# Optimization experiments

Measured on AMD Instinct MI355X. Metric: run time of the kernel, lower is better.

Reference implementation:

```python
import jax, jax.numpy as jnp
import numpy as np

D = 512      # d_model
S = 8        # num_quantum_states
B, T = 16, 1024
LN_EPS = 1e-5


def setup_inputs() -> dict:
    key = jax.random.key(0)
    ks = jax.random.split(key, 10)
    sc = lambda fan_in: 1.0 / np.sqrt(fan_in)
    return {
        "x": jax.random.normal(ks[0], (B, T, D), dtype=jnp.float32),
        # entanglement gates: torch Linear weight [out=D, in=2D], bias [D], stacked over S
        "W_ent": jax.random.uniform(ks[1], (S, D, 2 * D), minval=-sc(2 * D), maxval=sc(2 * D)),
        "b_ent": jax.random.uniform(ks[2], (S, D), minval=-sc(2 * D), maxval=sc(2 * D)),
        # measurement MLP: Linear(D*S->D), LayerNorm(D), Tanh, Linear(D->1)
        "m1_w": jax.random.uniform(ks[3], (D, D * S), minval=-sc(D * S), maxval=sc(D * S)),
        "m1_b": jax.random.uniform(ks[4], (D,), minval=-sc(D * S), maxval=sc(D * S)),
        "ln_g": jnp.ones((D,), dtype=jnp.float32),
        "ln_b": jnp.zeros((D,), dtype=jnp.float32),
        "m2_w": jax.random.uniform(ks[5], (1, D), minval=-sc(D), maxval=sc(D)),
        "m2_b": jax.random.uniform(ks[6], (1,), minval=-sc(D), maxval=sc(D)),
    }


def _layernorm(h, g, b):
    mu = jnp.mean(h, axis=-1, keepdims=True)
    var = jnp.mean(jnp.square(h - mu), axis=-1, keepdims=True)
    return (h - mu) * jax.lax.rsqrt(var + LN_EPS) * g + b


def reference(x, W_ent, b_ent, m1_w, m1_b, ln_g, ln_b, m2_w, m2_b):
    b_, t_, d_ = x.shape
    s_ = W_ent.shape[0]
    # gate(cat[x_i, x_j]).mean(dim=2) == x_i @ W1^T + mean_j(x_j) @ W2^T + b  (exact algebra)
    W1 = W_ent[:, :, :d_]   # [S, D, D] acts on x_i
    W2 = W_ent[:, :, d_:]   # [S, D, D] acts on x_j (mean over j)
    xbar = jnp.mean(x, axis=1)                                   # [B, D]
    ent = (jnp.einsum('btd,sed->bste', x, W1)                    # [B, S, T, D]
           + jnp.einsum('bd,sed->bse', xbar, W2)[:, :, None, :]
           + b_ent[None, :, None, :])
    # permute(0,2,3,1).reshape(B,T,D*S): feature layout is (d, s) fastest on s
    qv = jnp.transpose(ent, (0, 2, 3, 1)).reshape(b_, t_, d_ * s_)
    h = jnp.tanh(_layernorm(qv @ m1_w.T + m1_b, ln_g, ln_b))     # [B, T, D]
    attn_logits = h @ m2_w.T + m2_b                              # [B, T, 1]
    attn_weights = jax.nn.softmax(attn_logits, axis=1)
    context = jnp.sum(attn_weights * x, axis=1)                  # [B, D]
    return context, attn_weights
```

## Files before the change

### kernel.cpp

```cpp
#include <hip/hip_runtime.h>
#include <hip/hip_bf16.h>

typedef __attribute__((ext_vector_type(8))) short bf16x8;
typedef __attribute__((ext_vector_type(4))) float f32x4;

__device__ __forceinline__ float bf2f(unsigned short u) {
    union { unsigned int i; float f; } c; c.i = ((unsigned int)u) << 16; return c.f;
}
__device__ __forceinline__ unsigned short f2bf(float f) {
    union { float f; unsigned int i; } c; c.f = f;
    unsigned int x = c.i;
    x += 0x7fffu + ((x >> 16) & 1u);
    return (unsigned short)(x >> 16);
}
__device__ __forceinline__ unsigned int pk2(float a, float b) {
    __hip_bfloat162 h = __float22bfloat162_rn(float2{a, b});
    union { __hip_bfloat162 h; unsigned int u; } c; c.h = h; return c.u;
}
__device__ __forceinline__ float tanh_fast(float v) {
    float a = fabsf(v);
    a = fminf(a, 15.0f);
    float e = __expf(2.0f * a);
    float t = 1.0f - 2.0f / (e + 1.0f);
    return copysignf(t, v);
}

#define GLOAD_LDS16(gp, lp) \
    __builtin_amdgcn_global_load_lds((const __attribute__((address_space(1))) void*)(gp), \
                                     (__attribute__((address_space(3))) void*)(lp), 16, 0, 0)

#define MFMA(a, b, c) __builtin_amdgcn_mfma_f32_16x16x32_bf16((a), (b), (c), 0, 0, 0)

#define SBAR()  __builtin_amdgcn_s_barrier()
#define SCHED0() __builtin_amdgcn_sched_barrier(0)


__global__ void k_sumxp(const float* __restrict__ x, float* __restrict__ sumxp) {
    int b = blockIdx.x, tc = blockIdx.y;
    int tid = threadIdx.x;
    const float* xp = x + ((size_t)b * 1024 + tc * 64) * 512;
    float a0 = 0.f, a1 = 0.f;
    for (int t = 0; t < 64; ++t) {
        a0 += xp[(size_t)t * 512 + tid];
        a1 += xp[(size_t)t * 512 + tid + 256];
    }
    float* o = sumxp + (size_t)(b * 16 + tc) * 512;
    o[tid] = a0;
    o[tid + 256] = a1;
}

__global__ void k_prepA(const float* __restrict__ m1w, const float* __restrict__ bent,
                        unsigned short* __restrict__ Abf, float* __restrict__ bias2) {
    int i = blockIdx.x, tid = threadIdx.x;
    const float* row = m1w + (size_t)i * 4096;
    float acc = 0.f;
    #pragma unroll
    for (int q = 0; q < 4; ++q) {
        int col = q * 1024 + tid * 4;
        float4 v = *(const float4*)(row + col);
        ushort4 o;
        o.x = f2bf(v.x); o.y = f2bf(v.y); o.z = f2bf(v.z); o.w = f2bf(v.w);
        *(ushort4*)(Abf + (size_t)i * 4096 + col) = o;
        int e0 = col >> 3, s0 = col & 7;
        acc += v.x * bent[(s0    ) * 512 + e0];
        acc += v.y * bent[(s0 + 1) * 512 + e0];
        acc += v.z * bent[(s0 + 2) * 512 + e0];
        acc += v.w * bent[(s0 + 3) * 512 + e0];
    }
    #pragma unroll
    for (int off = 32; off; off >>= 1) acc += __shfl_xor(acc, off);
    __shared__ float r4[4];
    if ((tid & 63) == 0) r4[tid >> 6] = acc;
    __syncthreads();
    if (tid == 0) bias2[i] = r4[0] + r4[1] + r4[2] + r4[3];
}

__global__ void k_conv_W(const float* __restrict__ W, unsigned short* __restrict__ WT) {
    __shared__ float tile[128][33];
    int e0 = blockIdx.x * 16;
    int j0 = blockIdx.y * 32;
    int tid = threadIdx.x;
    int tx = tid & 31, ty = tid >> 5;
    #pragma unroll
    for (int q = 0; q < 16; ++q) {
        int lk = q * 8 + ty;
        int de = lk >> 3, s = lk & 7;
        int r = s * 512 + e0 + de;
        tile[lk][tx] = W[(size_t)r * 1024 + j0 + tx];
    }
    __syncthreads();
    int j = tid >> 3, ck = (tid & 7) * 16;
    unsigned short* dst = WT + (size_t)(j0 + j) * 4096 + e0 * 8 + ck;
    #pragma unroll
    for (int g = 0; g < 4; ++g) {
        ushort4 o;
        o.x = f2bf(tile[ck + g * 4 + 0][j]);
        o.y = f2bf(tile[ck + g * 4 + 1][j]);
        o.z = f2bf(tile[ck + g * 4 + 2][j]);
        o.w = f2bf(tile[ck + g * 4 + 3][j]);
        *(ushort4*)(dst + g * 4) = o;
    }
}

__launch_bounds__(512, 2)
__global__ void k_gemm1(const unsigned short* __restrict__ Abf,
                        const unsigned short* __restrict__ WT,
                        float* __restrict__ CpL, float* __restrict__ CpR) {
    __shared__ __align__(16) unsigned short sA[2][64 * 64];
    __shared__ __align__(16) unsigned short sB[2][256 * 64];
    int i0 = blockIdx.x * 64;
    int j0 = blockIdx.y * 256;
    int kbase = blockIdx.z * 512;
    int tid = threadIdx.x, lane = tid & 63, w = tid >> 6;
    int wm = w >> 2, wn = w & 3;
    int lr = lane >> 3, sl = lane & 7;
    int lo = lane & 15, hi = lane >> 4;
    int arow = w * 8 + lr;
    const unsigned short* gA = Abf + (size_t)(i0 + arow) * 4096 + kbase + ((sl ^ lr) << 3);
    const unsigned short* gB0 = WT + (size_t)(j0 + w * 32 + 0 * 8 + lr) * 4096 + kbase + ((sl ^ lr) << 3);
    const unsigned short* gB1 = WT + (size_t)(j0 + w * 32 + 1 * 8 + lr) * 4096 + kbase + ((sl ^ lr) << 3);
    const unsigned short* gB2 = WT + (size_t)(j0 + w * 32 + 2 * 8 + lr) * 4096 + kbase + ((sl ^ lr) << 3);
    const unsigned short* gB3 = WT + (size_t)(j0 + w * 32 + 3 * 8 + lr) * 4096 + kbase + ((sl ^ lr) << 3);
    bool left = (blockIdx.y < 2);
    f32x4 acc[2][4] = {};

#define G1_STAGE(tt, bufn)                                                    \
    do {                                                                      \
        int koff = (tt) * 64;                                                 \
        GLOAD_LDS16(gA + koff, &sA[bufn][w * 8 * 64]);                        \
        GLOAD_LDS16(gB0 + koff, &sB[bufn][(w * 32 + 0) * 64]);                \
        GLOAD_LDS16(gB1 + koff, &sB[bufn][(w * 32 + 8) * 64]);                \
        GLOAD_LDS16(gB2 + koff, &sB[bufn][(w * 32 + 16) * 64]);               \
        GLOAD_LDS16(gB3 + koff, &sB[bufn][(w * 32 + 24) * 64]);               \
        SCHED0();                                                             \
    } while (0)

    G1_STAGE(0, 0);
    #pragma unroll
    for (int t = 0; t < 8; ++t) {
        int buf = t & 1;
        if (t < 7) {
            G1_STAGE(t + 1, buf ^ 1);
            asm volatile("s_waitcnt vmcnt(5)" ::: "memory");
        } else {
            asm volatile("s_waitcnt vmcnt(0)" ::: "memory");
        }
        SCHED0(); SBAR(); SCHED0();
        __builtin_amdgcn_s_setprio(1);
        #pragma unroll
        for (int kk = 0; kk < 2; ++kk) {
            int slotX = ((kk * 4 + hi) ^ (lo & 7)) << 3;
            bf16x8 a0 = *(const bf16x8*)(&sA[buf][(wm * 32 +      lo) * 64 + slotX]);
            bf16x8 a1 = *(const bf16x8*)(&sA[buf][(wm * 32 + 16 + lo) * 64 + slotX]);
            #pragma unroll
            for (int n = 0; n < 4; ++n) {
                bf16x8 bb = *(const bf16x8*)(&sB[buf][(wn * 64 + n * 16 + lo) * 64 + slotX]);
                if (left) {
                    acc[0][n] = MFMA(a0, bb, acc[0][n]);
                    acc[1][n] = MFMA(a1, bb, acc[1][n]);
                } else {
                    acc[0][n] = MFMA(bb, a0, acc[0][n]);
                    acc[1][n] = MFMA(bb, a1, acc[1][n]);
                }
            }
        }
        __builtin_amdgcn_s_setprio(0);
        if (t < 7) { SCHED0(); SBAR(); SCHED0(); }
    }
#undef G1_STAGE

    int ksoff = blockIdx.z * 262144;
    if (left) {
        #pragma unroll
        for (int m = 0; m < 2; ++m) {
            int ib = i0 + wm * 32 + m * 16 + hi * 4;
            #pragma unroll
            for (int n = 0; n < 4; ++n) {
                int j = j0 + wn * 64 + n * 16 + lo;
                #pragma unroll
                for (int r = 0; r < 4; ++r)
                    CpL[ksoff + (ib + r) * 512 + j] = acc[m][n][r];
            }
        }
    } else {
        #pragma unroll
        for (int m = 0; m < 2; ++m) {
            int ic = i0 + wm * 32 + m * 16 + lo;
            #pragma unroll
            for (int n = 0; n < 4; ++n) {
                int db = j0 - 512 + wn * 64 + n * 16 + hi * 4;
                #pragma unroll
                for (int r = 0; r < 4; ++r)
                    CpR[ksoff + (db + r) * 512 + ic] = acc[m][n][r];
            }
        }
    }
}

__global__ void k_reduce(const float* __restrict__ CpL, const float* __restrict__ CpR,
                         unsigned short* __restrict__ M1bf, unsigned short* __restrict__ M2t) {
    int bx = blockIdx.x;
    const float* Cp = (bx < 256) ? CpL : CpR;
    unsigned short* ob = (bx < 256) ? M1bf : M2t;
    int gid = (bx & 255) * 256 + threadIdx.x;
    float4 s = ((const float4*)Cp)[gid];
    #pragma unroll
    for (int ks = 1; ks < 8; ++ks) {
        float4 t = ((const float4*)Cp)[ks * 65536 + gid];
        s.x += t.x; s.y += t.y; s.z += t.z; s.w += t.w;
    }
    ushort4 o;
    o.x = f2bf(s.x); o.y = f2bf(s.y); o.z = f2bf(s.z); o.w = f2bf(s.w);
    ((ushort4*)ob)[gid] = o;
}

__global__ void k_cb(const float* __restrict__ sumxp, const unsigned short* __restrict__ M2t,
                     const float* __restrict__ bias2, const float* __restrict__ m1b,
                     float* __restrict__ cbo) {
    int b = blockIdx.x, i0 = blockIdx.y * 64;
    int tid = threadIdx.x;
    __shared__ float sSx[512];
    for (int d = tid; d < 512; d += 256) {
        float s = 0.f;
        #pragma unroll
        for (int p = 0; p < 16; ++p)
            s += sumxp[(size_t)(b * 16 + p) * 512 + d];
        sSx[d] = s;
    }
    __syncthreads();
    int il = tid & 63, dq = tid >> 6;
    const unsigned short* mp = M2t + (size_t)dq * 128 * 512 + i0 + il;
    float acc = 0.f;
    #pragma unroll 4
    for (int dd = 0; dd < 128; ++dd)
        acc += sSx[dq * 128 + dd] * bf2f(mp[(size_t)dd * 512]);
    __shared__ float sPart[4][64];
    sPart[dq][il] = acc;
    __syncthreads();
    if (tid < 64) {
        float v = sPart[0][tid] + sPart[1][tid] + sPart[2][tid] + sPart[3][tid];
        cbo[b * 512 + i0 + tid] = v * (1.0f / 1024.0f) + bias2[i0 + tid] + m1b[i0 + tid];
    }
}

__launch_bounds__(512)
__global__ void k_gemm2s(const float* __restrict__ x,
                         const unsigned short* __restrict__ M1bf,
                         unsigned short* __restrict__ ypk) {
    __shared__ __align__(16) unsigned short sA[64 * 64];
    __shared__ __align__(16) unsigned short sB[512 * 64];
    int bt0 = blockIdx.x * 64;
    int tid = threadIdx.x, lane = tid & 63, w = tid >> 6;
    int wm = w >> 2, wn = w & 3;
    int lo = lane & 15, hi = lane >> 4;
    int lr = lane >> 3, sl = lane & 7;
    int arow = tid >> 3, aslot = tid & 7;
    const float* gA = x + (size_t)(bt0 + arow) * 512 + aslot * 8;
    unsigned short* dAp = sA + arow * 64 + ((aslot ^ (arow & 7)) << 3);
    const unsigned short* gB[8];
    #pragma unroll
    for (int g = 0; g < 8; ++g)
        gB[g] = M1bf + (size_t)(w * 64 + g * 8 + lr) * 512 + ((sl ^ lr) << 3);
    f32x4 acc[2][8] = {};
    for (int k0 = 0; k0 < 512; k0 += 64) {
        if (k0) __syncthreads();
        #pragma unroll
        for (int g = 0; g < 8; ++g)
            GLOAD_LDS16(gB[g] + k0, &sB[(w * 64 + g * 8) * 64]);
        float4 f0 = *(const float4*)(gA + k0);
        float4 f1 = *(const float4*)(gA + k0 + 4);
        bf16x8 pk;
        pk[0] = (short)f2bf(f0.x); pk[1] = (short)f2bf(f0.y);
        pk[2] = (short)f2bf(f0.z); pk[3] = (short)f2bf(f0.w);
        pk[4] = (short)f2bf(f1.x); pk[5] = (short)f2bf(f1.y);
        pk[6] = (short)f2bf(f1.z); pk[7] = (short)f2bf(f1.w);
        *(bf16x8*)dAp = pk;
        __syncthreads();
        #pragma unroll
        for (int kk = 0; kk < 2; ++kk) {
            int slotX = ((kk * 4 + hi) ^ (lo & 7)) << 3;
            bf16x8 a0 = *(const bf16x8*)(sA + (wm * 32 +      lo) * 64 + slotX);
            bf16x8 a1 = *(const bf16x8*)(sA + (wm * 32 + 16 + lo) * 64 + slotX);
            #pragma unroll
            for (int n = 0; n < 8; ++n) {
                bf16x8 bb = *(const bf16x8*)(sB + (wn * 128 + n * 16 + lo) * 64 + slotX);
                acc[0][n] = MFMA(a0, bb, acc[0][n]);
                acc[1][n] = MFMA(a1, bb, acc[1][n]);
            }
        }
    }
    unsigned short* yb = ypk + (size_t)blockIdx.x * 32768;
    #pragma unroll
    for (int m = 0; m < 2; ++m) {
        #pragma unroll
        for (int n = 0; n < 8; ++n) {
            unsigned int u0 = pk2(acc[m][n][0], acc[m][n][1]);
            unsigned int u1 = pk2(acc[m][n][2], acc[m][n][3]);
            uint2 o; o.x = u0; o.y = u1;
            *(uint2*)(yb + (((w * 16 + m * 8 + n) << 8) + (lane << 2))) = o;
        }
    }
}

__launch_bounds__(512)
__global__ void k_lnlogit(const unsigned short* __restrict__ ypk,
                          const float* __restrict__ cb,
                          const float* __restrict__ lng, const float* __restrict__ lnb,
                          const float* __restrict__ m2w, const float* __restrict__ m2b,
                          float* __restrict__ logits) {
    __shared__ __align__(16) unsigned short sY[32768];
    __shared__ float sCb[512], sG[512], sBe[512], sW[512];
    __shared__ float sS1[64][8], sS2[64][8], sLg[64][8];
    int blk = blockIdx.x;
    int bt0 = blk * 64;
    int b = bt0 >> 10;
    int tid = threadIdx.x, w = tid >> 6, lane = tid & 63;
    sCb[tid] = cb[b * 512 + tid];
    sG[tid]  = lng[tid];
    sBe[tid] = lnb[tid];
    sW[tid]  = m2w[tid];
    const unsigned short* src = ypk + (size_t)blk * 32768;
    #pragma unroll
    for (int it = 0; it < 8; ++it) {
        int off = (w * 8 + it) * 512;
        GLOAD_LDS16(src + off + (lane << 3), &sY[off]);
    }
    asm volatile("s_waitcnt vmcnt(0)" ::: "memory");
    __syncthreads();

    int row = tid >> 3, sub = tid & 7;
    int wm = row >> 5, m = (row >> 4) & 1, hi = (row >> 2) & 3, r = row & 3;
    float s1 = 0.f, s2 = 0.f;
    #pragma unroll
    for (int wn = 0; wn < 4; ++wn) {
        #pragma unroll
        for (int n = 0; n < 8; ++n) {
            int c = (wm * 4 + wn) * 16 + m * 8 + n;
            int eb = c * 256 + r;
            int ib = wn * 128 + n * 16;
            #pragma unroll
            for (int l2 = 0; l2 < 2; ++l2) {
                int lo = sub * 2 + l2;
                float v = bf2f(sY[eb + (hi * 16 + lo) * 4]) + sCb[ib + lo];
                s1 += v; s2 += v * v;
            }
        }
    }
    sS1[row][sub] = s1; sS2[row][sub] = s2;
    __syncthreads();
    float a1 = 0.f, a2 = 0.f;
    #pragma unroll
    for (int q = 0; q < 8; ++q) { a1 += sS1[row][q]; a2 += sS2[row][q]; }
    float mu = a1 * (1.0f / 512.0f);
    float var = a2 * (1.0f / 512.0f) - mu * mu;
    float rs = rsqrtf(var + 1e-5f);
    float lg = 0.f;
    #pragma unroll
    for (int wn = 0; wn < 4; ++wn) {
        #pragma unroll
        for (int n = 0; n < 8; ++n) {
            int c = (wm * 4 + wn) * 16 + m * 8 + n;
            int eb = c * 256 + r;
            int ib = wn * 128 + n * 16;
            #pragma unroll
            for (int l2 = 0; l2 < 2; ++l2) {
                int lo = sub * 2 + l2;
                float v = bf2f(sY[eb + (hi * 16 + lo) * 4]) + sCb[ib + lo];
                float h = tanh_fast((v - mu) * rs * sG[ib + lo] + sBe[ib + lo]);
                lg += h * sW[ib + lo];
            }
        }
    }
    sLg[row][sub] = lg;
    __syncthreads();
    if (sub == 0) {
        float t = 0.f;
        #pragma unroll
        for (int q = 0; q < 8; ++q) t += sLg[row][q];
        logits[bt0 + row] = t + m2b[0];
    }
}

__global__ void k_swctx(const float* __restrict__ x, const float* __restrict__ logits,
                        float* __restrict__ ctxp, float* __restrict__ attn) {
    int b = blockIdx.x, tc = blockIdx.y;
    int tid = threadIdx.x;
    __shared__ float red[4];
    __shared__ float sWt[1024];
    float4 v = ((const float4*)(logits + b * 1024))[tid];
    float mx = fmaxf(fmaxf(v.x, v.y), fmaxf(v.z, v.w));
    for (int off = 32; off; off >>= 1) mx = fmaxf(mx, __shfl_xor(mx, off));
    if ((tid & 63) == 0) red[tid >> 6] = mx;
    __syncthreads();
    mx = fmaxf(fmaxf(red[0], red[1]), fmaxf(red[2], red[3]));
    float e0 = expf(v.x - mx), e1 = expf(v.y - mx), e2 = expf(v.z - mx), e3 = expf(v.w - mx);
    float sm = e0 + e1 + e2 + e3;
    for (int off = 32; off; off >>= 1) sm += __shfl_xor(sm, off);
    __syncthreads();
    if ((tid & 63) == 0) red[tid >> 6] = sm;
    __syncthreads();
    float inv = 1.0f / (red[0] + red[1] + red[2] + red[3]);
    float4 o; o.x = e0 * inv; o.y = e1 * inv; o.z = e2 * inv; o.w = e3 * inv;
    ((float4*)sWt)[tid] = o;
    if (tc == 0) ((float4*)(attn + b * 1024))[tid] = o;
    __syncthreads();
    const float* xp = x + ((size_t)b * 1024 + tc * 64) * 512;
    const float* wp = sWt + tc * 64;
    float a0 = 0.f, a1 = 0.f;
    for (int t = 0; t < 64; ++t) {
        float wv = wp[t];
        a0 += wv * xp[(size_t)t * 512 + tid];
        a1 += wv * xp[(size_t)t * 512 + tid + 256];
    }
    float* op = ctxp + (size_t)(b * 16 + tc) * 512;
    op[tid] = a0;
    op[tid + 256] = a1;
}

__global__ void k_ctxred(const float* __restrict__ ctxp, float* __restrict__ ctx) {
    int idx = blockIdx.x * 256 + threadIdx.x;
    int b = idx >> 9, d = idx & 511;
    float s = 0.f;
    #pragma unroll
    for (int p = 0; p < 16; ++p)
        s += ctxp[(size_t)(b * 16 + p) * 512 + d];
    ctx[b * 512 + d] = s;
}

extern "C" void kernel_launch(void* const* d_in, const int* in_sizes, int n_in,
                              void* d_out, int out_size, void* d_ws, size_t ws_size,
                              hipStream_t stream) {
    (void)in_sizes; (void)n_in; (void)out_size; (void)ws_size;
    const float* x    = (const float*)d_in[0];
    const float* Went = (const float*)d_in[1];
    const float* bent = (const float*)d_in[2];
    const float* m1w  = (const float*)d_in[3];
    const float* m1b  = (const float*)d_in[4];
    const float* lng  = (const float*)d_in[5];
    const float* lnb  = (const float*)d_in[6];
    const float* m2w  = (const float*)d_in[7];
    const float* m2b  = (const float*)d_in[8];
    float* out = (float*)d_out;
    char* ws = (char*)d_ws;

    unsigned short* Abf   = (unsigned short*)(ws);
    unsigned short* WT    = (unsigned short*)(ws + 4194304);
    float* CpL            = (float*)(ws + 12582912);
    float* CpR            = (float*)(ws + 20971520);
    unsigned short* ypk   = (unsigned short*)(ws + 12582912);
    unsigned short* M1bf  = (unsigned short*)(ws + 29360128);
    unsigned short* M2t   = (unsigned short*)(ws + 29884416);
    float* sumxp  = (float*)(ws + 30408704);
    float* ctxp   = (float*)(ws + 30932992);
    float* bias2  = (float*)(ws + 31457280);
    float* cb     = (float*)(ws + 31459328);
    float* logits = (float*)(ws + 31492096);

    k_sumxp<<<dim3(16, 16), 256, 0, stream>>>(x, sumxp);
    k_prepA<<<512, 256, 0, stream>>>(m1w, bent, Abf, bias2);
    k_conv_W<<<dim3(32, 32), 256, 0, stream>>>(Went, WT);
    k_gemm1<<<dim3(8, 4, 8), 512, 0, stream>>>(Abf, WT, CpL, CpR);
    k_reduce<<<512, 256, 0, stream>>>(CpL, CpR, M1bf, M2t);
    k_cb<<<dim3(16, 8), 256, 0, stream>>>(sumxp, M2t, bias2, m1b, cb);
    k_gemm2s<<<256, 512, 0, stream>>>(x, M1bf, ypk);
    k_lnlogit<<<256, 512, 0, stream>>>(ypk, cb, lng, lnb, m2w, m2b, logits);
    k_swctx<<<dim3(16, 16), 256, 0, stream>>>(x, logits, ctxp, out + 8192);
    k_ctxred<<<32, 256, 0, stream>>>(ctxp, out);
}
```

Measured before the change: 92.74 us.

## Merge prep and reduce kernels, shrink gemm2 and LN tiles to 32 rows

Merges the three preprocessing kernels into one launch dispatched by block ID. The split-K reduce and the context-bias kernel become one kernel, and that kernel now reads the fp32 partials directly instead of a separate bf16 M2t buffer. The gemm2 and layernorm-logit kernels drop to 32-row tiles with 256 threads, doubling the grid to 512 blocks for better CU coverage. The intent is to cut launch count and raise occupancy, at the cost of the cb kernel doing eight times more strided fp32 reads.

```diff
diff --git a/kernel.cpp b/kernel.cpp
--- a/kernel.cpp
+++ b/kernel.cpp
@@ -34,71 +34,71 @@
 #define SBAR()  __builtin_amdgcn_s_barrier()
 #define SCHED0() __builtin_amdgcn_sched_barrier(0)
 
-
-__global__ void k_sumxp(const float* __restrict__ x, float* __restrict__ sumxp) {
-    int b = blockIdx.x, tc = blockIdx.y;
+__global__ void k_pre(const float* __restrict__ x, const float* __restrict__ m1w,
+                      const float* __restrict__ bent, const float* __restrict__ W,
+                      float* __restrict__ sumxp, unsigned short* __restrict__ Abf,
+                      float* __restrict__ bias2, unsigned short* __restrict__ WT) {
+    __shared__ float tile[128][33];
+    __shared__ float r4[4];
+    int bid = blockIdx.x;
     int tid = threadIdx.x;
-    const float* xp = x + ((size_t)b * 1024 + tc * 64) * 512;
-    float a0 = 0.f, a1 = 0.f;
-    for (int t = 0; t < 64; ++t) {
-        a0 += xp[(size_t)t * 512 + tid];
-        a1 += xp[(size_t)t * 512 + tid + 256];
-    }
-    float* o = sumxp + (size_t)(b * 16 + tc) * 512;
-    o[tid] = a0;
-    o[tid + 256] = a1;
-}
-
-__global__ void k_prepA(const float* __restrict__ m1w, const float* __restrict__ bent,
-                        unsigned short* __restrict__ Abf, float* __restrict__ bias2) {
-    int i = blockIdx.x, tid = threadIdx.x;
-    const float* row = m1w + (size_t)i * 4096;
-    float acc = 0.f;
-    #pragma unroll
-    for (int q = 0; q < 4; ++q) {
-        int col = q * 1024 + tid * 4;
-        float4 v = *(const float4*)(row + col);
-        ushort4 o;
-        o.x = f2bf(v.x); o.y = f2bf(v.y); o.z = f2bf(v.z); o.w = f2bf(v.w);
-        *(ushort4*)(Abf + (size_t)i * 4096 + col) = o;
-        int e0 = col >> 3, s0 = col & 7;
-        acc += v.x * bent[(s0    ) * 512 + e0];
-        acc += v.y * bent[(s0 + 1) * 512 + e0];
-        acc += v.z * bent[(s0 + 2) * 512 + e0];
-        acc += v.w * bent[(s0 + 3) * 512 + e0];
-    }
-    #pragma unroll
-    for (int off = 32; off; off >>= 1) acc += __shfl_xor(acc, off);
-    __shared__ float r4[4];
-    if ((tid & 63) == 0) r4[tid >> 6] = acc;
-    __syncthreads();
-    if (tid == 0) bias2[i] = r4[0] + r4[1] + r4[2] + r4[3];
-}
-
-__global__ void k_conv_W(const float* __restrict__ W, unsigned short* __restrict__ WT) {
-    __shared__ float tile[128][33];
-    int e0 = blockIdx.x * 16;
-    int j0 = blockIdx.y * 32;
-    int tid = threadIdx.x;
-    int tx = tid & 31, ty = tid >> 5;
-    #pragma unroll
-    for (int q = 0; q < 16; ++q) {
-        int lk = q * 8 + ty;
-        int de = lk >> 3, s = lk & 7;
-        int r = s * 512 + e0 + de;
-        tile[lk][tx] = W[(size_t)r * 1024 + j0 + tx];
-    }
-    __syncthreads();
-    int j = tid >> 3, ck = (tid & 7) * 16;
-    unsigned short* dst = WT + (size_t)(j0 + j) * 4096 + e0 * 8 + ck;
-    #pragma unroll
-    for (int g = 0; g < 4; ++g) {
-        ushort4 o;
-        o.x = f2bf(tile[ck + g * 4 + 0][j]);
-        o.y = f2bf(tile[ck + g * 4 + 1][j]);
-        o.z = f2bf(tile[ck + g * 4 + 2][j]);
-        o.w = f2bf(tile[ck + g * 4 + 3][j]);
-        *(ushort4*)(dst + g * 4) = o;
+    if (bid < 256) {
+        int b = bid >> 4, tc = bid & 15;
+        const float* xp = x + ((size_t)b * 1024 + tc * 64) * 512;
+        float a0 = 0.f, a1 = 0.f;
+        for (int t = 0; t < 64; ++t) {
+            a0 += xp[(size_t)t * 512 + tid];
+            a1 += xp[(size_t)t * 512 + tid + 256];
+        }
+        float* o = sumxp + (size_t)(b * 16 + tc) * 512;
+        o[tid] = a0;
+        o[tid + 256] = a1;
+    } else if (bid < 768) {
+        int i = bid - 256;
+        const float* row = m1w + (size_t)i * 4096;
+        float acc = 0.f;
+        #pragma unroll
+        for (int q = 0; q < 4; ++q) {
+            int col = q * 1024 + tid * 4;
+            float4 v = *(const float4*)(row + col);
+            ushort4 o;
+            o.x = f2bf(v.x); o.y = f2bf(v.y); o.z = f2bf(v.z); o.w = f2bf(v.w);
+            *(ushort4*)(Abf + (size_t)i * 4096 + col) = o;
+            int e0 = col >> 3, s0 = col & 7;
+            acc += v.x * bent[(s0    ) * 512 + e0];
+            acc += v.y * bent[(s0 + 1) * 512 + e0];
+            acc += v.z * bent[(s0 + 2) * 512 + e0];
+            acc += v.w * bent[(s0 + 3) * 512 + e0];
+        }
+        #pragma unroll
+        for (int off = 32; off; off >>= 1) acc += __shfl_xor(acc, off);
+        if ((tid & 63) == 0) r4[tid >> 6] = acc;
+        __syncthreads();
+        if (tid == 0) bias2[i] = r4[0] + r4[1] + r4[2] + r4[3];
+    } else {
+        int idx = bid - 768;
+        int e0 = (idx & 31) * 16;
+        int j0 = (idx >> 5) * 32;
+        int tx = tid & 31, ty = tid >> 5;
+        #pragma unroll
+        for (int q = 0; q < 16; ++q) {
+            int lk = q * 8 + ty;
+            int de = lk >> 3, s = lk & 7;
+            int r = s * 512 + e0 + de;
+            tile[lk][tx] = W[(size_t)r * 1024 + j0 + tx];
+        }
+        __syncthreads();
+        int j = tid >> 3, ck = (tid & 7) * 16;
+        unsigned short* dst = WT + (size_t)(j0 + j) * 4096 + e0 * 8 + ck;
+        #pragma unroll
+        for (int g = 0; g < 4; ++g) {
+            ushort4 o;
+            o.x = f2bf(tile[ck + g * 4 + 0][j]);
+            o.y = f2bf(tile[ck + g * 4 + 1][j]);
+            o.z = f2bf(tile[ck + g * 4 + 2][j]);
+            o.w = f2bf(tile[ck + g * 4 + 3][j]);
+            *(ushort4*)(dst + g * 4) = o;
+        }
     }
 }
 
@@ -197,76 +197,77 @@
     }
 }
 
-__global__ void k_reduce(const float* __restrict__ CpL, const float* __restrict__ CpR,
-                         unsigned short* __restrict__ M1bf, unsigned short* __restrict__ M2t) {
-    int bx = blockIdx.x;
-    const float* Cp = (bx < 256) ? CpL : CpR;
-    unsigned short* ob = (bx < 256) ? M1bf : M2t;
-    int gid = (bx & 255) * 256 + threadIdx.x;
-    float4 s = ((const float4*)Cp)[gid];
-    #pragma unroll
-    for (int ks = 1; ks < 8; ++ks) {
-        float4 t = ((const float4*)Cp)[ks * 65536 + gid];
-        s.x += t.x; s.y += t.y; s.z += t.z; s.w += t.w;
-    }
-    ushort4 o;
-    o.x = f2bf(s.x); o.y = f2bf(s.y); o.z = f2bf(s.z); o.w = f2bf(s.w);
-    ((ushort4*)ob)[gid] = o;
-}
-
-__global__ void k_cb(const float* __restrict__ sumxp, const unsigned short* __restrict__ M2t,
-                     const float* __restrict__ bias2, const float* __restrict__ m1b,
-                     float* __restrict__ cbo) {
-    int b = blockIdx.x, i0 = blockIdx.y * 64;
+__global__ void k_mid(const float* __restrict__ CpL, const float* __restrict__ CpR,
+                      const float* __restrict__ sumxp, const float* __restrict__ bias2,
+                      const float* __restrict__ m1b,
+                      unsigned short* __restrict__ M1bf, float* __restrict__ cbo) {
+    __shared__ float sSx[512];
+    __shared__ float sPart[4][64];
+    int bid = blockIdx.x;
     int tid = threadIdx.x;
-    __shared__ float sSx[512];
-    for (int d = tid; d < 512; d += 256) {
-        float s = 0.f;
-        #pragma unroll
-        for (int p = 0; p < 16; ++p)
-            s += sumxp[(size_t)(b * 16 + p) * 512 + d];
-        sSx[d] = s;
-    }
-    __syncthreads();
-    int il = tid & 63, dq = tid >> 6;
-    const unsigned short* mp = M2t + (size_t)dq * 128 * 512 + i0 + il;
-    float acc = 0.f;
-    #pragma unroll 4
-    for (int dd = 0; dd < 128; ++dd)
-        acc += sSx[dq * 128 + dd] * bf2f(mp[(size_t)dd * 512]);
-    __shared__ float sPart[4][64];
-    sPart[dq][il] = acc;
-    __syncthreads();
-    if (tid < 64) {
-        float v = sPart[0][tid] + sPart[1][tid] + sPart[2][tid] + sPart[3][tid];
-        cbo[b * 512 + i0 + tid] = v * (1.0f / 1024.0f) + bias2[i0 + tid] + m1b[i0 + tid];
-    }
-}
-
-__launch_bounds__(512)
+    if (bid < 256) {
+        int gid = bid * 256 + tid;
+        float4 s = ((const float4*)CpL)[gid];
+        #pragma unroll
+        for (int ks = 1; ks < 8; ++ks) {
+            float4 t = ((const float4*)CpL)[ks * 65536 + gid];
+            s.x += t.x; s.y += t.y; s.z += t.z; s.w += t.w;
+        }
+        ushort4 o;
+        o.x = f2bf(s.x); o.y = f2bf(s.y); o.z = f2bf(s.z); o.w = f2bf(s.w);
+        ((ushort4*)M1bf)[gid] = o;
+    } else {
+        int bb = bid - 256;
+        int b = bb >> 3, i0 = (bb & 7) * 64;
+        for (int d = tid; d < 512; d += 256) {
+            float s = 0.f;
+            #pragma unroll
+            for (int p = 0; p < 16; ++p)
+                s += sumxp[(size_t)(b * 16 + p) * 512 + d];
+            sSx[d] = s;
+        }
+        __syncthreads();
+        int il = tid & 63, dq = tid >> 6;
+        float acc = 0.f;
+        #pragma unroll 1
+        for (int ks = 0; ks < 8; ++ks) {
+            const float* cp = CpR + (size_t)ks * 262144 + (size_t)(dq * 128) * 512 + i0 + il;
+            #pragma unroll 4
+            for (int dd = 0; dd < 128; ++dd)
+                acc += sSx[dq * 128 + dd] * cp[(size_t)dd * 512];
+        }
+        sPart[dq][il] = acc;
+        __syncthreads();
+        if (tid < 64) {
+            float v = sPart[0][tid] + sPart[1][tid] + sPart[2][tid] + sPart[3][tid];
+            cbo[b * 512 + i0 + tid] = v * (1.0f / 1024.0f) + bias2[i0 + tid] + m1b[i0 + tid];
+        }
+    }
+}
+
+__launch_bounds__(256, 2)
 __global__ void k_gemm2s(const float* __restrict__ x,
                          const unsigned short* __restrict__ M1bf,
                          unsigned short* __restrict__ ypk) {
-    __shared__ __align__(16) unsigned short sA[64 * 64];
+    __shared__ __align__(16) unsigned short sA[32 * 64];
     __shared__ __align__(16) unsigned short sB[512 * 64];
-    int bt0 = blockIdx.x * 64;
+    int bt0 = blockIdx.x * 32;
     int tid = threadIdx.x, lane = tid & 63, w = tid >> 6;
-    int wm = w >> 2, wn = w & 3;
     int lo = lane & 15, hi = lane >> 4;
     int lr = lane >> 3, sl = lane & 7;
     int arow = tid >> 3, aslot = tid & 7;
     const float* gA = x + (size_t)(bt0 + arow) * 512 + aslot * 8;
     unsigned short* dAp = sA + arow * 64 + ((aslot ^ (arow & 7)) << 3);
-    const unsigned short* gB[8];
-    #pragma unroll
-    for (int g = 0; g < 8; ++g)
-        gB[g] = M1bf + (size_t)(w * 64 + g * 8 + lr) * 512 + ((sl ^ lr) << 3);
+    const unsigned short* gB[16];
+    #pragma unroll
+    for (int g = 0; g < 16; ++g)
+        gB[g] = M1bf + (size_t)(w * 128 + g * 8 + lr) * 512 + ((sl ^ lr) << 3);
     f32x4 acc[2][8] = {};
     for (int k0 = 0; k0 < 512; k0 += 64) {
         if (k0) __syncthreads();
         #pragma unroll
-        for (int g = 0; g < 8; ++g)
-            GLOAD_LDS16(gB[g] + k0, &sB[(w * 64 + g * 8) * 64]);
+        for (int g = 0; g < 16; ++g)
+            GLOAD_LDS16(gB[g] + k0, &sB[(w * 128 + g * 8) * 64]);
         float4 f0 = *(const float4*)(gA + k0);
         float4 f1 = *(const float4*)(gA + k0 + 4);
         bf16x8 pk;
@@ -279,17 +280,17 @@
         #pragma unroll
         for (int kk = 0; kk < 2; ++kk) {
             int slotX = ((kk * 4 + hi) ^ (lo & 7)) << 3;
-            bf16x8 a0 = *(const bf16x8*)(sA + (wm * 32 +      lo) * 64 + slotX);
-            bf16x8 a1 = *(const bf16x8*)(sA + (wm * 32 + 16 + lo) * 64 + slotX);
+            bf16x8 a0 = *(const bf16x8*)(sA + (     lo) * 64 + slotX);
+            bf16x8 a1 = *(const bf16x8*)(sA + (16 + lo) * 64 + slotX);
             #pragma unroll
             for (int n = 0; n < 8; ++n) {
-                bf16x8 bb = *(const bf16x8*)(sB + (wn * 128 + n * 16 + lo) * 64 + slotX);
+                bf16x8 bb = *(const bf16x8*)(sB + (w * 128 + n * 16 + lo) * 64 + slotX);
                 acc[0][n] = MFMA(a0, bb, acc[0][n]);
                 acc[1][n] = MFMA(a1, bb, acc[1][n]);
             }
         }
     }
-    unsigned short* yb = ypk + (size_t)blockIdx.x * 32768;
+    unsigned short* yb = ypk + (size_t)blockIdx.x * 16384;
     #pragma unroll
     for (int m = 0; m < 2; ++m) {
         #pragma unroll
@@ -297,29 +298,33 @@
             unsigned int u0 = pk2(acc[m][n][0], acc[m][n][1]);
             unsigned int u1 = pk2(acc[m][n][2], acc[m][n][3]);
             uint2 o; o.x = u0; o.y = u1;
-            *(uint2*)(yb + (((w * 16 + m * 8 + n) << 8) + (lane << 2))) = o;
-        }
-    }
-}
-
-__launch_bounds__(512)
+            *(uint2*)(yb + ((((w * 2 + m) * 8 + n) << 8) + (lane << 2))) = o;
+        }
+    }
+}
+
+__launch_bounds__(256)
 __global__ void k_lnlogit(const unsigned short* __restrict__ ypk,
                           const float* __restrict__ cb,
                           const float* __restrict__ lng, const float* __restrict__ lnb,
                           const float* __restrict__ m2w, const float* __restrict__ m2b,
                           float* __restrict__ logits) {
-    __shared__ __align__(16) unsigned short sY[32768];
+    __shared__ __align__(16) unsigned short sY[16384];
     __shared__ float sCb[512], sG[512], sBe[512], sW[512];
-    __shared__ float sS1[64][8], sS2[64][8], sLg[64][8];
+    __shared__ float sS1[32][8], sS2[32][8], sLg[32][8];
     int blk = blockIdx.x;
-    int bt0 = blk * 64;
+    int bt0 = blk * 32;
     int b = bt0 >> 10;
     int tid = threadIdx.x, w = tid >> 6, lane = tid & 63;
-    sCb[tid] = cb[b * 512 + tid];
-    sG[tid]  = lng[tid];
-    sBe[tid] = lnb[tid];
-    sW[tid]  = m2w[tid];
-    const unsigned short* src = ypk + (size_t)blk * 32768;
+    #pragma unroll
+    for (int q = 0; q < 2; ++q) {
+        int c = q * 256 + tid;
+        sCb[c] = cb[b * 512 + c];
+        sG[c]  = lng[c];
+        sBe[c] = lnb[c];
+        sW[c]  = m2w[c];
+    }
+    const unsigned short* src = ypk + (size_t)blk * 16384;
     #pragma unroll
     for (int it = 0; it < 8; ++it) {
         int off = (w * 8 + it) * 512;
@@ -329,13 +334,13 @@
     __syncthreads();
 
     int row = tid >> 3, sub = tid & 7;
-    int wm = row >> 5, m = (row >> 4) & 1, hi = (row >> 2) & 3, r = row & 3;
+    int m = row >> 4, hi = (row >> 2) & 3, r = row & 3;
     float s1 = 0.f, s2 = 0.f;
     #pragma unroll
     for (int wn = 0; wn < 4; ++wn) {
         #pragma unroll
         for (int n = 0; n < 8; ++n) {
-            int c = (wm * 4 + wn) * 16 + m * 8 + n;
+            int c = (wn * 2 + m) * 8 + n;
             int eb = c * 256 + r;
             int ib = wn * 128 + n * 16;
             #pragma unroll
@@ -359,7 +364,7 @@
     for (int wn = 0; wn < 4; ++wn) {
         #pragma unroll
         for (int n = 0; n < 8; ++n) {
-            int c = (wm * 4 + wn) * 16 + m * 8 + n;
+            int c = (wn * 2 + m) * 8 + n;
             int eb = c * 256 + r;
             int ib = wn * 128 + n * 16;
             #pragma unroll
@@ -449,21 +454,17 @@
     float* CpR            = (float*)(ws + 20971520);
     unsigned short* ypk   = (unsigned short*)(ws + 12582912);
     unsigned short* M1bf  = (unsigned short*)(ws + 29360128);
-    unsigned short* M2t   = (unsigned short*)(ws + 29884416);
-    float* sumxp  = (float*)(ws + 30408704);
-    float* ctxp   = (float*)(ws + 30932992);
-    float* bias2  = (float*)(ws + 31457280);
-    float* cb     = (float*)(ws + 31459328);
-    float* logits = (float*)(ws + 31492096);
-
-    k_sumxp<<<dim3(16, 16), 256, 0, stream>>>(x, sumxp);
-    k_prepA<<<512, 256, 0, stream>>>(m1w, bent, Abf, bias2);
-    k_conv_W<<<dim3(32, 32), 256, 0, stream>>>(Went, WT);
+    float* sumxp  = (float*)(ws + 29884416);
+    float* ctxp   = (float*)(ws + 30408704);
+    float* bias2  = (float*)(ws + 30932992);
+    float* cb     = (float*)(ws + 30935040);
+    float* logits = (float*)(ws + 30967808);
+
+    k_pre<<<1792, 256, 0, stream>>>(x, m1w, bent, Went, sumxp, Abf, bias2, WT);
     k_gemm1<<<dim3(8, 4, 8), 512, 0, stream>>>(Abf, WT, CpL, CpR);
-    k_reduce<<<512, 256, 0, stream>>>(CpL, CpR, M1bf, M2t);
-    k_cb<<<dim3(16, 8), 256, 0, stream>>>(sumxp, M2t, bias2, m1b, cb);
-    k_gemm2s<<<256, 512, 0, stream>>>(x, M1bf, ypk);
-    k_lnlogit<<<256, 512, 0, stream>>>(ypk, cb, lng, lnb, m2w, m2b, logits);
+    k_mid<<<384, 256, 0, stream>>>(CpL, CpR, sumxp, bias2, m1b, M1bf, cb);
+    k_gemm2s<<<512, 256, 0, stream>>>(x, M1bf, ypk);
+    k_lnlogit<<<512, 256, 0, stream>>>(ypk, cb, lng, lnb, m2w, m2b, logits);
     k_swctx<<<dim3(16, 16), 256, 0, stream>>>(x, logits, ctxp, out + 8192);
     k_ctxred<<<32, 256, 0, stream>>>(ctxp, out);
 }
```

Measured after the change: 144.1 us. 1.55x slower.
